# Kernel optimization log

Measured on AMD Instinct MI355X. Metric: run time of the kernel, lower is better.

## Reference

```python
import jax, jax.numpy as jnp
import numpy as np

GRID = 7
COORD = 5.0
NO_OBJ = 0.5


def _corners(xywh, r, c):
    # xywh: [...,4] with (x_cell, y_cell, w, h); r,c broadcastable grid indices
    x, y, w, h = xywh[..., 0], xywh[..., 1], xywh[..., 2], xywh[..., 3]
    cx = (x + c) / GRID
    cy = (y + r) / GRID
    return cx - w / 2, cy - h / 2, cx + w / 2, cy + h / 2


def _iou(a, b):
    ax1, ay1, ax2, ay2 = a
    bx1, by1, bx2, by2 = b
    iw = jnp.maximum(jnp.minimum(ax2, bx2) - jnp.maximum(ax1, bx1), 0.0)
    ih = jnp.maximum(jnp.minimum(ay2, by2) - jnp.maximum(ay1, by1), 0.0)
    inter = iw * ih
    area_a = (ax2 - ax1) * (ay2 - ay1)
    area_b = (bx2 - bx1) * (by2 - by1)
    union = area_a + area_b - inter
    return jnp.where(union > 0, inter / jnp.where(union > 0, union, 1.0), 0.0)


def setup_inputs() -> dict:
    key = jax.random.key(0)
    k1, k2, k3 = jax.random.split(key, 3)
    B = 8192
    data = jax.random.uniform(k1, (B, GRID, GRID, 30), dtype=jnp.float32)
    labels = jax.random.uniform(k2, (B, GRID, GRID, 30), dtype=jnp.float32)
    # obj flag at channel 4 must be exactly 1 for obj cells
    obj = jax.random.randint(k3, (B, GRID, GRID), 0, 2).astype(jnp.float32)
    labels = labels.at[..., 4].set(obj)
    return {"data": data, "labels": labels}


def reference(data, labels):
    B = data.shape[0]
    r = jnp.arange(GRID, dtype=data.dtype)[None, :, None]  # row index -> y offset
    c = jnp.arange(GRID, dtype=data.dtype)[None, None, :]  # col index -> x offset

    box1 = _corners(data[..., 0:4], r, c)
    box2 = _corners(data[..., 5:9], r, c)
    gt = _corners(labels[..., 0:4], r, c)

    iou1 = _iou(box1, gt)  # [B,7,7]
    iou2 = _iou(box2, gt)
    resp1 = iou1 >= iou2

    xy1 = jnp.sum((data[..., 0:2] - labels[..., 0:2]) ** 2, -1)
    xy2 = jnp.sum((data[..., 5:7] - labels[..., 5:7]) ** 2, -1)
    wh1 = jnp.sum((jnp.sqrt(data[..., 2:4]) - jnp.sqrt(labels[..., 2:4])) ** 2, -1)
    wh2 = jnp.sum((jnp.sqrt(data[..., 7:9]) - jnp.sqrt(labels[..., 7:9])) ** 2, -1)

    d4, d9 = data[..., 4], data[..., 9]
    co = COORD * jnp.where(resp1, xy1, xy2)
    wh = COORD * jnp.where(resp1, wh1, wh2)
    confi = jnp.where(resp1, (d4 - iou1) ** 2, (d9 - iou2) ** 2)
    noobj_in = NO_OBJ * jnp.where(resp1, d9 ** 2, d4 ** 2)
    cls = jnp.sum((data[..., 10:] - labels[..., 10:]) ** 2, -1)

    m = (labels[..., 4] == 1).astype(data.dtype)
    obj_loss = m * (co + wh + confi + noobj_in + cls)
    noobj_loss = (1.0 - m) * NO_OBJ * (d4 ** 2 + d9 ** 2)
    return jnp.sum(obj_loss + noobj_loss) / B
```

## Files before the change

kernel.cpp:

```cpp
#include <hip/hip_runtime.h>

#define COORD 5.0f
#define NO_OBJ 0.5f
#define NCELLS (8192 * 49)
#define INV_B (1.0f / 8192.0f)

#define CPB 128
#define FPB (CPB * 30)
#define NBLK (NCELLS / CPB)

__device__ __forceinline__ float iou_calc(float ax1, float ay1, float ax2, float ay2,
                                          float bx1, float by1, float bx2, float by2) {
    float iw = fminf(ax2, bx2) - fmaxf(ax1, bx1);
    iw = fmaxf(iw, 0.0f);
    float ih = fminf(ay2, by2) - fmaxf(ay1, by1);
    ih = fmaxf(ih, 0.0f);
    float inter = iw * ih;
    float area_a = (ax2 - ax1) * (ay2 - ay1);
    float area_b = (bx2 - bx1) * (by2 - by1);
    float uni = area_a + area_b - inter;
    return uni > 0.0f ? inter / uni : 0.0f;
}

__global__ __launch_bounds__(128) void yolo_loss_kernel(
    const float* __restrict__ data, const float* __restrict__ labels,
    float* __restrict__ ws) {
    __shared__ float sd[FPB];
    __shared__ float sl[FPB];

    const int tid = threadIdx.x;
    const size_t fbase = (size_t)blockIdx.x * FPB;

    const float4* gd4 = (const float4*)(data + fbase);
    const float4* gl4 = (const float4*)(labels + fbase);
    float4* sd4 = (float4*)sd;
    float4* sl4 = (float4*)sl;
#pragma unroll
    for (int j = 0; j < 7; j++) {
        sd4[j * 128 + tid] = gd4[j * 128 + tid];
        sl4[j * 128 + tid] = gl4[j * 128 + tid];
    }
    {
        const float2* gd2 = (const float2*)(data + fbase + 3584);
        const float2* gl2 = (const float2*)(labels + fbase + 3584);
        ((float2*)(sd + 3584))[tid] = gd2[tid];
        ((float2*)(sl + 3584))[tid] = gl2[tid];
    }
    __syncthreads();

    const int idx = blockIdx.x * CPB + tid;
    const int cell = idx % 49;
    const float r = (float)(cell / 7);
    const float c = (float)(cell % 7);

    float d[30], l[30];
    const float2* dp = (const float2*)(sd + tid * 30);
    const float2* lp = (const float2*)(sl + tid * 30);
#pragma unroll
    for (int i = 0; i < 15; i++) {
        float2 v = dp[i];
        d[2 * i] = v.x; d[2 * i + 1] = v.y;
        float2 w2 = lp[i];
        l[2 * i] = w2.x; l[2 * i + 1] = w2.y;
    }

    const float inv_g = 1.0f / 7.0f;
    float cx1 = (d[0] + c) * inv_g, cy1 = (d[1] + r) * inv_g;
    float b1x1 = cx1 - d[2] * 0.5f, b1y1 = cy1 - d[3] * 0.5f;
    float b1x2 = cx1 + d[2] * 0.5f, b1y2 = cy1 + d[3] * 0.5f;
    float cx2 = (d[5] + c) * inv_g, cy2 = (d[6] + r) * inv_g;
    float b2x1 = cx2 - d[7] * 0.5f, b2y1 = cy2 - d[8] * 0.5f;
    float b2x2 = cx2 + d[7] * 0.5f, b2y2 = cy2 + d[8] * 0.5f;
    float gx = (l[0] + c) * inv_g, gy = (l[1] + r) * inv_g;
    float gx1 = gx - l[2] * 0.5f, gy1 = gy - l[3] * 0.5f;
    float gx2 = gx + l[2] * 0.5f, gy2 = gy + l[3] * 0.5f;

    float iou1 = iou_calc(b1x1, b1y1, b1x2, b1y2, gx1, gy1, gx2, gy2);
    float iou2 = iou_calc(b2x1, b2y1, b2x2, b2y2, gx1, gy1, gx2, gy2);
    bool resp1 = iou1 >= iou2;

    float xy1 = (d[0] - l[0]) * (d[0] - l[0]) + (d[1] - l[1]) * (d[1] - l[1]);
    float xy2 = (d[5] - l[5]) * (d[5] - l[5]) + (d[6] - l[6]) * (d[6] - l[6]);
    float s2 = sqrtf(d[2]) - sqrtf(l[2]);
    float s3 = sqrtf(d[3]) - sqrtf(l[3]);
    float wh1 = s2 * s2 + s3 * s3;
    float s7 = sqrtf(d[7]) - sqrtf(l[7]);
    float s8 = sqrtf(d[8]) - sqrtf(l[8]);
    float wh2 = s7 * s7 + s8 * s8;

    float d4 = d[4], d9 = d[9];
    float co = COORD * (resp1 ? xy1 : xy2);
    float wh = COORD * (resp1 ? wh1 : wh2);
    float ci = resp1 ? (d4 - iou1) * (d4 - iou1) : (d9 - iou2) * (d9 - iou2);
    float noobj_in = NO_OBJ * (resp1 ? d9 * d9 : d4 * d4);
    float cls = 0.0f;
#pragma unroll
    for (int i = 10; i < 30; i++) {
        float t = d[i] - l[i];
        cls += t * t;
    }

    float loss = (l[4] == 1.0f)
                     ? (co + wh + ci + noobj_in + cls)
                     : NO_OBJ * (d4 * d4 + d9 * d9);
    float acc = loss * INV_B;

#pragma unroll
    for (int off = 32; off > 0; off >>= 1)
        acc += __shfl_down(acc, off, 64);

    __shared__ float wsum[2];
    if ((tid & 63) == 0) wsum[tid >> 6] = acc;
    __syncthreads();
    if (tid == 0) ws[blockIdx.x] = wsum[0] + wsum[1];
}

__global__ __launch_bounds__(256) void reduce_kernel(const float* __restrict__ ws,
                                                     float* __restrict__ out) {
    float s = 0.0f;
    for (int i = threadIdx.x; i < NBLK; i += 256) s += ws[i];
#pragma unroll
    for (int off = 32; off > 0; off >>= 1)
        s += __shfl_down(s, off, 64);
    __shared__ float w[4];
    if ((threadIdx.x & 63) == 0) w[threadIdx.x >> 6] = s;
    __syncthreads();
    if (threadIdx.x == 0) out[0] = w[0] + w[1] + w[2] + w[3];
}

extern "C" void kernel_launch(void* const* d_in, const int* in_sizes, int n_in,
                              void* d_out, int out_size, void* d_ws, size_t ws_size,
                              hipStream_t stream) {
    const float* data = (const float*)d_in[0];
    const float* labels = (const float*)d_in[1];
    float* out = (float*)d_out;
    float* ws = (float*)d_ws;

    yolo_loss_kernel<<<NBLK, CPB, 0, stream>>>(data, labels, ws);
    reduce_kernel<<<1, 256, 0, stream>>>(ws, out);
}
```

Baseline: 115.4 us.

## Process two tiles per block with register-prefetch of the second tile

Each block now handles two 128-cell tiles. While the first tile's loss is computed from shared memory, the global loads for the second tile are already issued into registers, then written to shared memory after a barrier. This is meant to overlap memory latency with compute and halve the number of blocks and partial sums. It adds register pressure from holding the prefetched float4s alongside the per-thread 60-float arrays, which could reduce occupancy.

```diff
diff --git a/kernel.cpp b/kernel.cpp
--- a/kernel.cpp
+++ b/kernel.cpp
@@ -6,8 +6,8 @@
 #define INV_B (1.0f / 8192.0f)
 
 #define CPB 128
-#define FPB (CPB * 30)
-#define NBLK (NCELLS / CPB)
+#define FPT (CPB * 30)
+#define NBLK (NCELLS / (CPB * 2))
 
 __device__ __forceinline__ float iou_calc(float ax1, float ay1, float ax2, float ay2,
                                           float bx1, float by1, float bx2, float by2) {
@@ -22,33 +22,9 @@
     return uni > 0.0f ? inter / uni : 0.0f;
 }
 
-__global__ __launch_bounds__(128) void yolo_loss_kernel(
-    const float* __restrict__ data, const float* __restrict__ labels,
-    float* __restrict__ ws) {
-    __shared__ float sd[FPB];
-    __shared__ float sl[FPB];
-
-    const int tid = threadIdx.x;
-    const size_t fbase = (size_t)blockIdx.x * FPB;
-
-    const float4* gd4 = (const float4*)(data + fbase);
-    const float4* gl4 = (const float4*)(labels + fbase);
-    float4* sd4 = (float4*)sd;
-    float4* sl4 = (float4*)sl;
-#pragma unroll
-    for (int j = 0; j < 7; j++) {
-        sd4[j * 128 + tid] = gd4[j * 128 + tid];
-        sl4[j * 128 + tid] = gl4[j * 128 + tid];
-    }
-    {
-        const float2* gd2 = (const float2*)(data + fbase + 3584);
-        const float2* gl2 = (const float2*)(labels + fbase + 3584);
-        ((float2*)(sd + 3584))[tid] = gd2[tid];
-        ((float2*)(sl + 3584))[tid] = gl2[tid];
-    }
-    __syncthreads();
-
-    const int idx = blockIdx.x * CPB + tid;
+__device__ __forceinline__ float cell_loss(const float* __restrict__ sd,
+                                           const float* __restrict__ sl,
+                                           int idx, int tid) {
     const int cell = idx % 49;
     const float r = (float)(cell / 7);
     const float c = (float)(cell % 7);
@@ -100,10 +76,73 @@
         cls += t * t;
     }
 
-    float loss = (l[4] == 1.0f)
-                     ? (co + wh + ci + noobj_in + cls)
-                     : NO_OBJ * (d4 * d4 + d9 * d9);
-    float acc = loss * INV_B;
+    return (l[4] == 1.0f) ? (co + wh + ci + noobj_in + cls)
+                          : NO_OBJ * (d4 * d4 + d9 * d9);
+}
+
+__global__ __launch_bounds__(CPB) void yolo_loss_kernel(
+    const float* __restrict__ data, const float* __restrict__ labels,
+    float* __restrict__ ws) {
+    __shared__ float sd[FPT];
+    __shared__ float sl[FPT];
+
+    const int tid = threadIdx.x;
+    const size_t base0 = (size_t)blockIdx.x * (2 * FPT);
+
+    float4* sd4 = (float4*)sd;
+    float4* sl4 = (float4*)sl;
+
+    float4 pd[7], pl[7];
+    float2 pd2, pl2;
+
+    {
+        const float4* gd4 = (const float4*)(data + base0);
+        const float4* gl4 = (const float4*)(labels + base0);
+#pragma unroll
+        for (int j = 0; j < 7; j++) {
+            pd[j] = gd4[j * 128 + tid];
+            pl[j] = gl4[j * 128 + tid];
+        }
+        pd2 = ((const float2*)(data + base0 + 3584))[tid];
+        pl2 = ((const float2*)(labels + base0 + 3584))[tid];
+    }
+#pragma unroll
+    for (int j = 0; j < 7; j++) {
+        sd4[j * 128 + tid] = pd[j];
+        sl4[j * 128 + tid] = pl[j];
+    }
+    ((float2*)(sd + 3584))[tid] = pd2;
+    ((float2*)(sl + 3584))[tid] = pl2;
+    __syncthreads();
+
+    {
+        const float4* gd4 = (const float4*)(data + base0 + FPT);
+        const float4* gl4 = (const float4*)(labels + base0 + FPT);
+#pragma unroll
+        for (int j = 0; j < 7; j++) {
+            pd[j] = gd4[j * 128 + tid];
+            pl[j] = gl4[j * 128 + tid];
+        }
+        pd2 = ((const float2*)(data + base0 + FPT + 3584))[tid];
+        pl2 = ((const float2*)(labels + base0 + FPT + 3584))[tid];
+    }
+
+    const int idx0 = blockIdx.x * (2 * CPB) + tid;
+    float acc = cell_loss(sd, sl, idx0, tid);
+
+    __syncthreads();
+
+#pragma unroll
+    for (int j = 0; j < 7; j++) {
+        sd4[j * 128 + tid] = pd[j];
+        sl4[j * 128 + tid] = pl[j];
+    }
+    ((float2*)(sd + 3584))[tid] = pd2;
+    ((float2*)(sl + 3584))[tid] = pl2;
+    __syncthreads();
+
+    acc += cell_loss(sd, sl, idx0 + CPB, tid);
+    acc *= INV_B;
 
 #pragma unroll
     for (int off = 32; off > 0; off >>= 1)
```

Result: slower. 143.1 us (+24.0%).
